# Optimization experiments

Measured on AMD Instinct MI355X. Metric: run time of the kernel, lower is better.

## Reference

```python
import jax, jax.numpy as jnp
import numpy as np

B, S, E, H = 4, 4096, 1024, 16
D = E // H  # head_dim = 64
EPS = 1e-6


def setup_inputs() -> dict:
    key = jax.random.key(0)
    ks = jax.random.split(key, 11)
    inv = 1.0 / np.sqrt(E)
    return {
        "query": jax.random.normal(ks[0], (B, S, E), dtype=jnp.float32),
        "key": jax.random.normal(ks[1], (B, S, E), dtype=jnp.float32),
        "value": jax.random.normal(ks[2], (B, S, E), dtype=jnp.float32),
        "key_padding_mask": jnp.zeros((B, S), dtype=bool),
        "Wq": jax.random.uniform(ks[3], (E, E), jnp.float32, -inv, inv),
        "bq": jnp.zeros((E,), jnp.float32),
        "Wk": jax.random.uniform(ks[4], (E, E), jnp.float32, -inv, inv),
        "bk": jnp.zeros((E,), jnp.float32),
        "Wv": jax.random.uniform(ks[5], (E, E), jnp.float32, -inv, inv),
        "bv": jnp.zeros((E,), jnp.float32),
        "Wo": jax.random.uniform(ks[6], (E, E), jnp.float32, -inv, inv),
        "bo": jnp.zeros((E,), jnp.float32),
    }


def _heads(x):
    # (B,S,E) -> (B,H,S,D)
    return x.reshape(B, -1, H, D).transpose(0, 2, 1, 3)


def reference(query, key, value, key_padding_mask, Wq, bq, Wk, bk, Wv, bv, Wo, bo):
    q = _heads(query @ Wq.T + bq)
    k = _heads(key @ Wk.T + bk)
    v = _heads(value @ Wv.T + bv)

    q_aug = jax.nn.relu(q) + EPS
    k_aug = jax.nn.relu(k) + EPS
    # mask out padded keys: (B,S_k) -> (B,1,S_k,1)
    k_aug = jnp.where(key_padding_mask[:, None, :, None], 0.0, k_aug)

    kv_context = jnp.einsum("bhsd,bhsv->bhdv", k_aug, v)  # (B,H,D,D)
    k_sum = k_aug.sum(axis=2)                                # (B,H,D)
    denom = jnp.einsum("bhqd,bhd->bhq", q_aug, k_sum)
    denom = jnp.maximum(denom, EPS)

    attn = jnp.einsum("bhqd,bhdv->bhqv", q_aug, kv_context) / denom[..., None]
    attn = attn.transpose(0, 2, 1, 3).reshape(B, -1, E)      # (B,S_q,E)
    # dropout is identity in eval mode
    return attn @ Wo.T + bo
```

## Files before the change

### kernel.cpp

```cpp
#include <hip/hip_runtime.h>
#include <hip/hip_bf16.h>
#include <stdint.h>

#define B_ 4
#define S_ 4096
#define E_ 1024
#define H_ 16
#define D_ 64
#define M_ (B_*S_)
constexpr float kEPS = 1e-6f;

typedef unsigned short u16;
typedef unsigned char  u8;
typedef __bf16 bf16x8 __attribute__((ext_vector_type(8)));
typedef float  f32x4  __attribute__((ext_vector_type(4)));
typedef u16    u16x8  __attribute__((ext_vector_type(8)));

typedef const __attribute__((address_space(1))) void* gaddr_t;
typedef __attribute__((address_space(3))) void*       laddr_t;

__device__ __forceinline__ u16 f2bf(float f) {
    union { float f; uint32_t u; } v; v.f = f;
    uint32_t u = v.u;
    u += 0x7fffu + ((u >> 16) & 1u);
    return (u16)(u >> 16);
}
__device__ __forceinline__ float hi2f(uint32_t d) {
    union { uint32_t u; float f; } v; v.u = d & 0xffff0000u;
    return v.f;
}
__device__ __forceinline__ float lo2f(uint32_t d) {
    union { uint32_t u; float f; } v; v.u = d << 16;
    return v.f;
}

#define VM_WAIT(n) asm volatile("s_waitcnt vmcnt(" #n ")" ::: "memory")
#define LG0        asm volatile("s_waitcnt lgkmcnt(0)" ::: "memory")
#define SBAR       asm volatile("s_barrier" ::: "memory")

__global__ __launch_bounds__(256)
void cvt3_kernel(const float* __restrict__ s0, const float* __restrict__ s1,
                 const float* __restrict__ s2,
                 u16* __restrict__ d0, u16* __restrict__ d1, u16* __restrict__ d2,
                 int n4)
{
    const int z = blockIdx.y;
    const float* src = (z == 0) ? s0 : (z == 1) ? s1 : s2;
    u16*         dst = (z == 0) ? d0 : (z == 1) ? d1 : d2;
    const int stride = gridDim.x * blockDim.x;
    for (int i = blockIdx.x * blockDim.x + threadIdx.x; i < n4; i += stride) {
        float4 v = reinterpret_cast<const float4*>(src)[i];
        ushort4 o;
        o.x = f2bf(v.x); o.y = f2bf(v.y); o.z = f2bf(v.z); o.w = f2bf(v.w);
        reinterpret_cast<ushort4*>(dst)[i] = o;
    }
}

__global__ __launch_bounds__(256)
void cvtw_kernel(const float* __restrict__ w0, const float* __restrict__ w1,
                 const float* __restrict__ w2, const float* __restrict__ w3,
                 u16* __restrict__ o0, u16* __restrict__ o1,
                 u16* __restrict__ o2, u16* __restrict__ o3)
{
    const int z = blockIdx.y;
    const float* src = (z == 0) ? w0 : (z == 1) ? w1 : (z == 2) ? w2 : w3;
    u16*         dst = (z == 0) ? o0 : (z == 1) ? o1 : (z == 2) ? o2 : o3;
    const int i = blockIdx.x * blockDim.x + threadIdx.x;
    float4 v = reinterpret_cast<const float4*>(src)[i];
    ushort4 o;
    o.x = f2bf(v.x); o.y = f2bf(v.y); o.z = f2bf(v.z); o.w = f2bf(v.w);
    reinterpret_cast<ushort4*>(dst)[i] = o;
}

#define BM2 256
#define BN2 128
#define BKT2 32
#define NT2 (E_/BKT2)

struct QKVArgs {
    const u16*   A[3];
    const u16*   W[3];
    const float* bias[3];
    const u8*    mask;
    u16*         C[3];
};

template<bool MERGED>
__global__ __launch_bounds__(512, 4)
void gemm2b(QKVArgs qa,
            const u16* __restrict__ A1, const u16* __restrict__ Bw1,
            const float* __restrict__ bias1, float* __restrict__ Cf)
{
    extern __shared__ u16 lds[];
    const int tid  = threadIdx.x;
    const int wid  = tid >> 6, lane = tid & 63;
    const int wqr  = wid >> 1, wqc = wid & 1;
    const int m0   = blockIdx.x * BM2;
    const int n0   = blockIdx.y * BN2;
    const int fr   = lane & 15;
    const int cg   = lane >> 4;

    const u16* A;  const u16* Bw;  const float* bias;  u16* Cb;  int epi;
    if constexpr (MERGED) {
        const int z = blockIdx.z;
        A = qa.A[z]; Bw = qa.W[z]; bias = qa.bias[z]; Cb = qa.C[z]; epi = z + 1;
    } else {
        A = A1; Bw = Bw1; bias = bias1; Cb = nullptr; epi = 0;
    }

    const int srow = tid >> 2;
    const int skey = (srow ^ (srow >> 2)) & 3;
    const int sck  = (tid & 3) ^ skey;
    const u16* aS0 = A  + (size_t)(m0 + srow)*E_        + sck*8;
    const u16* aS1 = A  + (size_t)(m0 + 128 + srow)*E_  + sck*8;
    const u16* bS0 = Bw + (size_t)(n0 + srow)*E_        + sck*8;

    const int lkey = (fr ^ (fr >> 2)) & 3;
    const int kxr  = (cg ^ lkey) * 8;
    int arow[4], brow[4];
#pragma unroll
    for (int mf = 0; mf < 4; ++mf) arow[mf] = (wqr*64 + mf*16 + fr)*32 + kxr;
#pragma unroll
    for (int nf = 0; nf < 4; ++nf) brow[nf] = 8192 + (wqc*64 + nf*16 + fr)*32 + kxr;

    f32x4 acc[4][4] = {};

    float bias_v[4];
#pragma unroll
    for (int nf = 0; nf < 4; ++nf) bias_v[nf] = bias[n0 + wqc*64 + nf*16 + fr];

#define STAGE(BUF, T) do { \
        const size_t ko_ = (size_t)(T) * BKT2; \
        u16* ab_ = lds + (BUF)*12288; \
        __builtin_amdgcn_global_load_lds((gaddr_t)(aS0 + ko_), (laddr_t)(ab_ + tid*8),          16, 0, 0); \
        __builtin_amdgcn_global_load_lds((gaddr_t)(aS1 + ko_), (laddr_t)(ab_ + (tid+512)*8),    16, 0, 0); \
        __builtin_amdgcn_global_load_lds((gaddr_t)(bS0 + ko_), (laddr_t)(ab_ + 8192 + tid*8),   16, 0, 0); \
    } while (0)

    STAGE(0, 0);
    VM_WAIT(0);
    SBAR;
    __builtin_amdgcn_sched_barrier(0);

#pragma unroll 1
    for (int T = 0; T < NT2; ++T) {
        const int cb = T & 1;
        const u16* buf = lds + cb*12288;
        bf16x8 afr[4], bfv[4];
#pragma unroll
        for (int mf = 0; mf < 4; ++mf) afr[mf] = *reinterpret_cast<const bf16x8*>(buf + arow[mf]);
#pragma unroll
        for (int nf = 0; nf < 4; ++nf) bfv[nf] = *reinterpret_cast<const bf16x8*>(buf + brow[nf]);
        if (T < NT2 - 1) STAGE(cb ^ 1, T + 1);
        LG0;
        __builtin_amdgcn_sched_barrier(0);
        __builtin_amdgcn_s_setprio(1);
#pragma unroll
        for (int mf = 0; mf < 4; ++mf)
#pragma unroll
            for (int nf = 0; nf < 4; ++nf)
                acc[mf][nf] = __builtin_amdgcn_mfma_f32_16x16x32_bf16(afr[mf], bfv[nf], acc[mf][nf], 0, 0, 0);
        __builtin_amdgcn_s_setprio(0);
        VM_WAIT(0);
        SBAR;
        __builtin_amdgcn_sched_barrier(0);
    }
#undef STAGE

    const int bblk = m0 >> 12;
    const int sloc = m0 & 4095;
#pragma unroll
    for (int mf = 0; mf < 4; ++mf) {
#pragma unroll
        for (int nf = 0; nf < 4; ++nf) {
            const int gn = n0 + wqc*64 + nf*16 + fr;
            const int mb = wqr*64 + mf*16 + cg*4;
            if (epi >= 2) {
                ushort4 o;
#pragma unroll
                for (int r = 0; r < 4; ++r) {
                    float x = acc[mf][nf][r] + bias_v[nf];
                    if (epi == 2) {
                        x = fmaxf(x, 0.f) + kEPS;
                        if (qa.mask[m0 + mb + r]) x = 0.f;
                    }
                    ((u16*)&o)[r] = f2bf(x);
                }
                *reinterpret_cast<ushort4*>(Cb + ((size_t)(bblk*1024 + gn))*4096 + sloc + mb) = o;
            } else if (epi == 1) {
#pragma unroll
                for (int r = 0; r < 4; ++r) {
                    const int gm = m0 + mb + r;
                    float x = acc[mf][nf][r] + bias_v[nf];
                    x = fmaxf(x, 0.f) + kEPS;
                    Cb[(size_t)gm*E_ + gn] = f2bf(x);
                }
            } else {
#pragma unroll
                for (int r = 0; r < 4; ++r) {
                    const int gm = m0 + mb + r;
                    Cf[(size_t)gm*E_ + gn] = acc[mf][nf][r] + bias_v[nf];
                }
            }
        }
    }
}

#define NSC 8
#define KCH (S_/NSC)
__global__ __launch_bounds__(256)
void kv_mfma_kernel(const u16* __restrict__ KaT, const u16* __restrict__ VvT,
                    float* __restrict__ kvp, float* __restrict__ ksp)
{
    __shared__ float sm[4][64];
    const int bh = blockIdx.x, sc = blockIdx.y;
    const int tid = threadIdx.x;
    const int w = tid >> 6, lane = tid & 63;
    const int fr = lane & 15, cg = lane >> 4;

    const u16* Ar = VvT + ((size_t)bh*64 + w*16 + fr)*4096 + sc*KCH;
    const u16* Br0 = KaT + ((size_t)bh*64 + fr)*4096 + sc*KCH;

    f32x4 acc[4] = {};
#pragma unroll 2
    for (int ks = 0; ks < KCH/32; ++ks) {
        const int ko = ks*32 + cg*8;
        bf16x8 af = *reinterpret_cast<const bf16x8*>(Ar + ko);
#pragma unroll
        for (int nf = 0; nf < 4; ++nf) {
            bf16x8 bf = *reinterpret_cast<const bf16x8*>(Br0 + (size_t)nf*16*4096 + ko);
            acc[nf] = __builtin_amdgcn_mfma_f32_16x16x32_bf16(af, bf, acc[nf], 0, 0, 0);
        }
    }
    float* dst = kvp + ((size_t)sc*64 + bh)*4096;
#pragma unroll
    for (int nf = 0; nf < 4; ++nf)
#pragma unroll
        for (int r = 0; r < 4; ++r)
            dst[(w*16 + cg*4 + r)*64 + nf*16 + fr] = acc[nf][r];

    {
        const int d = tid & 63, qq = tid >> 6;
        const u16* kr = KaT + ((size_t)bh*64 + d)*4096 + sc*KCH + qq*(KCH/4);
        float s = 0.f;
#pragma unroll 4
        for (int i = 0; i < KCH/4/8; ++i) {
            bf16x8 kk = *reinterpret_cast<const bf16x8*>(kr + i*8);
#pragma unroll
            for (int j = 0; j < 8; ++j) s += (float)kk[j];
        }
        sm[qq][d] = s;
    }
    __syncthreads();
    if (tid < 64)
        ksp[((size_t)sc*64 + bh)*64 + tid] = sm[0][tid] + sm[1][tid] + sm[2][tid] + sm[3][tid];
}

__global__ __launch_bounds__(256)
void kv_reduce_kernel(const float* __restrict__ kvp, const float* __restrict__ ksp,
                      u16* __restrict__ kvT, float* __restrict__ ksum)
{
    const int i = blockIdx.x*256 + threadIdx.x;
    float s = 0.f;
#pragma unroll
    for (int c = 0; c < NSC; ++c) s += kvp[(size_t)c*262144 + i];
    kvT[i] = f2bf(s);
    if (i < 4096) {
        float t = 0.f;
#pragma unroll
        for (int c = 0; c < NSC; ++c) t += ksp[(size_t)c*4096 + i];
        ksum[i] = t;
    }
}

__global__ __launch_bounds__(256)
void attn_kernel(const u16* __restrict__ Qa, const u16* __restrict__ kvT,
                 const float* __restrict__ ksum, u16* __restrict__ attn)
{
    __shared__ u16  Qs[256*64];
    __shared__ u16  Ts[64*64];
    __shared__ float kss[64];
    __shared__ float invd[256];

    const int bh = blockIdx.x, b = bh >> 4, h = bh & 15;
    const int s0 = blockIdx.y * 256;
    const int tid = threadIdx.x;
    const int wid = tid >> 6, lane = tid & 63;
    const int fr = lane & 15, cg = lane >> 4;

#pragma unroll
    for (int j = 0; j < 8; ++j) {
        int L = (wid*8 + j)*64 + lane;
        int row = L >> 3, c = L & 7;
        int cs = c ^ (row & 7);
        const u16* src = Qa + (size_t)(b*S_ + s0 + row)*E_ + h*64 + cs*8;
        __builtin_amdgcn_global_load_lds((gaddr_t)src, (laddr_t)(Qs + L*8), 16, 0, 0);
    }
#pragma unroll
    for (int k = 0; k < 2; ++k) {
        int g = k*256 + tid;
        int v = g >> 3, c = g & 7;
        uint4 q = *reinterpret_cast<const uint4*>(kvT + (size_t)bh*4096 + g*8);
        int cs = c ^ (v & 7);
        *reinterpret_cast<uint4*>(Ts + v*64 + cs*8) = q;
    }
    if (tid < 64) kss[tid] = ksum[bh*64 + tid];
    asm volatile("s_waitcnt vmcnt(0) lgkmcnt(0)" ::: "memory");
    __syncthreads();

    {
        float den = 0.f;
#pragma unroll
        for (int c = 0; c < 8; ++c) {
            uint4 qc = *reinterpret_cast<const uint4*>(Qs + tid*64 + (c ^ (tid & 7))*8);
            den += lo2f(qc.x)*kss[c*8+0] + hi2f(qc.x)*kss[c*8+1]
                 + lo2f(qc.y)*kss[c*8+2] + hi2f(qc.y)*kss[c*8+3]
                 + lo2f(qc.z)*kss[c*8+4] + hi2f(qc.z)*kss[c*8+5]
                 + lo2f(qc.w)*kss[c*8+6] + hi2f(qc.w)*kss[c*8+7];
        }
        invd[tid] = 1.0f / fmaxf(den, kEPS);
    }
    __syncthreads();

    f32x4 acc[4][4] = {};
#pragma unroll
    for (int ks = 0; ks < 2; ++ks) {
        bf16x8 bfrag[4];
#pragma unroll
        for (int nf = 0; nf < 4; ++nf) {
            int v = nf*16 + fr;
            bfrag[nf] = *reinterpret_cast<const bf16x8*>(Ts + v*64 + ((ks*4 + cg) ^ (v & 7))*8);
        }
#pragma unroll
        for (int mf = 0; mf < 4; ++mf) {
            int m = wid*64 + mf*16 + fr;
            bf16x8 afrag = *reinterpret_cast<const bf16x8*>(Qs + m*64 + ((ks*4 + cg) ^ (m & 7))*8);
#pragma unroll
            for (int nf = 0; nf < 4; ++nf)
                acc[mf][nf] = __builtin_amdgcn_mfma_f32_16x16x32_bf16(afrag, bfrag[nf], acc[mf][nf], 0, 0, 0);
        }
    }

#pragma unroll
    for (int mf = 0; mf < 4; ++mf) {
#pragma unroll
        for (int nf = 0; nf < 4; ++nf) {
            const int v = nf*16 + fr;
#pragma unroll
            for (int r = 0; r < 4; ++r) {
                const int row = wid*64 + mf*16 + cg*4 + r;
                float x = acc[mf][nf][r] * invd[row];
                attn[(size_t)(b*S_ + s0 + row)*E_ + h*64 + v] = f2bf(x);
            }
        }
    }
}

extern "C" void kernel_launch(void* const* d_in, const int* in_sizes, int n_in,
                              void* d_out, int out_size, void* d_ws, size_t ws_size,
                              hipStream_t stream)
{
    const float* query = (const float*)d_in[0];
    const float* key   = (const float*)d_in[1];
    const float* value = (const float*)d_in[2];
    const u8*    mask  = (const u8*)d_in[3];
    const float* Wq = (const float*)d_in[4];
    const float* bq = (const float*)d_in[5];
    const float* Wk = (const float*)d_in[6];
    const float* bk = (const float*)d_in[7];
    const float* Wv = (const float*)d_in[8];
    const float* bv = (const float*)d_in[9];
    const float* Wo = (const float*)d_in[10];
    const float* bo = (const float*)d_in[11];
    float* out = (float*)d_out;

    const size_t SZ_ME = (size_t)M_ * E_;
    const size_t SZ_EE = (size_t)E_ * E_;

    char* ws = (char*)d_ws;
    u16* qx   = (u16*)ws; ws += SZ_ME*2;
    u16* kx   = (u16*)ws; ws += SZ_ME*2;
    u16* vx   = (u16*)ws; ws += SZ_ME*2;
    u16* Qa   = (u16*)ws; ws += SZ_ME*2;
    u16* KaT  = (u16*)ws; ws += SZ_ME*2;
    u16* VvT  = (u16*)ws; ws += SZ_ME*2;
    u16* wqb  = (u16*)ws; ws += SZ_EE*2;
    u16* wkb  = (u16*)ws; ws += SZ_EE*2;
    u16* wvb  = (u16*)ws; ws += SZ_EE*2;
    u16* wob  = (u16*)ws; ws += SZ_EE*2;
    float* kvp = (float*)ws; ws += (size_t)NSC*64*4096*4;
    float* ksp = (float*)ws; ws += (size_t)NSC*4096*4;
    u16*  kvT  = (u16*)ws;  ws += (size_t)64*4096*2;
    float* ksum= (float*)ws; ws += 4096*4;

    u16* attnb = qx;

    cvt3_kernel<<<dim3(2048, 3), 256, 0, stream>>>(query, key, value, qx, kx, vx, (int)(SZ_ME/4));
    cvtw_kernel<<<dim3(1024, 4), 256, 0, stream>>>(Wq, Wk, Wv, Wo, wqb, wkb, wvb, wob);

    QKVArgs qa;
    qa.A[0] = qx;  qa.A[1] = kx;  qa.A[2] = vx;
    qa.W[0] = wqb; qa.W[1] = wkb; qa.W[2] = wvb;
    qa.bias[0] = bq; qa.bias[1] = bk; qa.bias[2] = bv;
    qa.mask = mask;
    qa.C[0] = Qa; qa.C[1] = KaT; qa.C[2] = VvT;
    dim3 ggrid(M_/BM2, E_/BN2, 3);
    constexpr size_t LDS_BYTES = 2 * 12288 * sizeof(u16);
    gemm2b<true><<<ggrid, 512, LDS_BYTES, stream>>>(qa, nullptr, nullptr, nullptr, nullptr);

    kv_mfma_kernel<<<dim3(64, NSC), 256, 0, stream>>>(KaT, VvT, kvp, ksp);
    kv_reduce_kernel<<<1024, 256, 0, stream>>>(kvp, ksp, kvT, ksum);

    attn_kernel<<<dim3(B_*H_, S_/256), 256, 0, stream>>>(Qa, kvT, ksum, attnb);

    QKVArgs dummy = {};
    dummy.mask = mask;
    gemm2b<false><<<dim3(M_/BM2, E_/BN2, 1), 512, LDS_BYTES, stream>>>(dummy, attnb, wob, bo, out);
}
```

Measured before the change: 279.9 us.

## Retile projection GEMMs to 128x128 tiles with 64-deep K and 8-way swizzle

```diff
diff --git a/kernel.cpp b/kernel.cpp
--- a/kernel.cpp
+++ b/kernel.cpp
@@ -72,10 +72,10 @@
     reinterpret_cast<ushort4*>(dst)[i] = o;
 }
 
-#define BM2 256
-#define BN2 128
-#define BKT2 32
-#define NT2 (E_/BKT2)
+#define BM 128
+#define BN 128
+#define BKT 64
+#define NKT (E_/BKT)
 
 struct QKVArgs {
     const u16*   A[3];
@@ -86,17 +86,17 @@
 };
 
 template<bool MERGED>
-__global__ __launch_bounds__(512, 4)
-void gemm2b(QKVArgs qa,
-            const u16* __restrict__ A1, const u16* __restrict__ Bw1,
-            const float* __restrict__ bias1, float* __restrict__ Cf)
+__global__ __launch_bounds__(256, 2)
+void gemm128(QKVArgs qa,
+             const u16* __restrict__ A1, const u16* __restrict__ Bw1,
+             const float* __restrict__ bias1, float* __restrict__ Cf)
 {
     extern __shared__ u16 lds[];
     const int tid  = threadIdx.x;
     const int wid  = tid >> 6, lane = tid & 63;
     const int wqr  = wid >> 1, wqc = wid & 1;
-    const int m0   = blockIdx.x * BM2;
-    const int n0   = blockIdx.y * BN2;
+    const int m0   = blockIdx.x * BM;
+    const int n0   = blockIdx.y * BN;
     const int fr   = lane & 15;
     const int cg   = lane >> 4;
 
@@ -108,20 +108,21 @@
         A = A1; Bw = Bw1; bias = bias1; Cb = nullptr; epi = 0;
     }
 
-    const int srow = tid >> 2;
-    const int skey = (srow ^ (srow >> 2)) & 3;
-    const int sck  = (tid & 3) ^ skey;
-    const u16* aS0 = A  + (size_t)(m0 + srow)*E_        + sck*8;
-    const u16* aS1 = A  + (size_t)(m0 + 128 + srow)*E_  + sck*8;
-    const u16* bS0 = Bw + (size_t)(n0 + srow)*E_        + sck*8;
-
-    const int lkey = (fr ^ (fr >> 2)) & 3;
-    const int kxr  = (cg ^ lkey) * 8;
+    int srowj[4], sckj[4];
+#pragma unroll
+    for (int j = 0; j < 4; ++j) {
+        const int s = j*256 + tid;
+        srowj[j] = s >> 3;
+        sckj[j]  = (s & 7) ^ (srowj[j] & 7);
+    }
+
     int arow[4], brow[4];
 #pragma unroll
-    for (int mf = 0; mf < 4; ++mf) arow[mf] = (wqr*64 + mf*16 + fr)*32 + kxr;
-#pragma unroll
-    for (int nf = 0; nf < 4; ++nf) brow[nf] = 8192 + (wqc*64 + nf*16 + fr)*32 + kxr;
+    for (int mf = 0; mf < 4; ++mf) arow[mf] = (wqr*64 + mf*16 + fr)*64;
+#pragma unroll
+    for (int nf = 0; nf < 4; ++nf) brow[nf] = 8192 + (wqc*64 + nf*16 + fr)*64;
+    const int kx0 = ((cg)     ^ (fr & 7)) * 8;
+    const int kx1 = ((4 + cg) ^ (fr & 7)) * 8;
 
     f32x4 acc[4][4] = {};
 
@@ -130,11 +131,15 @@
     for (int nf = 0; nf < 4; ++nf) bias_v[nf] = bias[n0 + wqc*64 + nf*16 + fr];
 
 #define STAGE(BUF, T) do { \
-        const size_t ko_ = (size_t)(T) * BKT2; \
-        u16* ab_ = lds + (BUF)*12288; \
-        __builtin_amdgcn_global_load_lds((gaddr_t)(aS0 + ko_), (laddr_t)(ab_ + tid*8),          16, 0, 0); \
-        __builtin_amdgcn_global_load_lds((gaddr_t)(aS1 + ko_), (laddr_t)(ab_ + (tid+512)*8),    16, 0, 0); \
-        __builtin_amdgcn_global_load_lds((gaddr_t)(bS0 + ko_), (laddr_t)(ab_ + 8192 + tid*8),   16, 0, 0); \
+        const size_t ko_ = (size_t)(T) * BKT; \
+        u16* lb_ = lds + (BUF)*16384; \
+        _Pragma("unroll") \
+        for (int j_ = 0; j_ < 4; ++j_) { \
+            const u16* as_ = A  + (size_t)(m0 + srowj[j_])*E_ + ko_ + sckj[j_]*8; \
+            const u16* bs_ = Bw + (size_t)(n0 + srowj[j_])*E_ + ko_ + sckj[j_]*8; \
+            __builtin_amdgcn_global_load_lds((gaddr_t)as_, (laddr_t)(lb_ + (j_*256 + tid)*8),        16, 0, 0); \
+            __builtin_amdgcn_global_load_lds((gaddr_t)bs_, (laddr_t)(lb_ + 8192 + (j_*256 + tid)*8), 16, 0, 0); \
+        } \
     } while (0)
 
     STAGE(0, 0);
@@ -143,23 +148,31 @@
     __builtin_amdgcn_sched_barrier(0);
 
 #pragma unroll 1
-    for (int T = 0; T < NT2; ++T) {
+    for (int T = 0; T < NKT; ++T) {
         const int cb = T & 1;
-        const u16* buf = lds + cb*12288;
-        bf16x8 afr[4], bfv[4];
-#pragma unroll
-        for (int mf = 0; mf < 4; ++mf) afr[mf] = *reinterpret_cast<const bf16x8*>(buf + arow[mf]);
-#pragma unroll
-        for (int nf = 0; nf < 4; ++nf) bfv[nf] = *reinterpret_cast<const bf16x8*>(buf + brow[nf]);
-        if (T < NT2 - 1) STAGE(cb ^ 1, T + 1);
+        const u16* buf = lds + cb*16384;
+        bf16x8 afr[4][2], bfv[4][2];
+#pragma unroll
+        for (int mf = 0; mf < 4; ++mf) {
+            afr[mf][0] = *reinterpret_cast<const bf16x8*>(buf + arow[mf] + kx0);
+            afr[mf][1] = *reinterpret_cast<const bf16x8*>(buf + arow[mf] + kx1);
+        }
+#pragma unroll
+        for (int nf = 0; nf < 4; ++nf) {
+            bfv[nf][0] = *reinterpret_cast<const bf16x8*>(buf + brow[nf] + kx0);
+            bfv[nf][1] = *reinterpret_cast<const bf16x8*>(buf + brow[nf] + kx1);
+        }
+        if (T < NKT - 1) STAGE(cb ^ 1, T + 1);
         LG0;
         __builtin_amdgcn_sched_barrier(0);
         __builtin_amdgcn_s_setprio(1);
 #pragma unroll
         for (int mf = 0; mf < 4; ++mf)
 #pragma unroll
-            for (int nf = 0; nf < 4; ++nf)
-                acc[mf][nf] = __builtin_amdgcn_mfma_f32_16x16x32_bf16(afr[mf], bfv[nf], acc[mf][nf], 0, 0, 0);
+            for (int nf = 0; nf < 4; ++nf) {
+                acc[mf][nf] = __builtin_amdgcn_mfma_f32_16x16x32_bf16(afr[mf][0], bfv[nf][0], acc[mf][nf], 0, 0, 0);
+                acc[mf][nf] = __builtin_amdgcn_mfma_f32_16x16x32_bf16(afr[mf][1], bfv[nf][1], acc[mf][nf], 0, 0, 0);
+            }
         __builtin_amdgcn_s_setprio(0);
         VM_WAIT(0);
         SBAR;
@@ -404,9 +417,9 @@
     qa.bias[0] = bq; qa.bias[1] = bk; qa.bias[2] = bv;
     qa.mask = mask;
     qa.C[0] = Qa; qa.C[1] = KaT; qa.C[2] = VvT;
-    dim3 ggrid(M_/BM2, E_/BN2, 3);
-    constexpr size_t LDS_BYTES = 2 * 12288 * sizeof(u16);
-    gemm2b<true><<<ggrid, 512, LDS_BYTES, stream>>>(qa, nullptr, nullptr, nullptr, nullptr);
+    dim3 ggrid(M_/BM, E_/BN, 3);
+    constexpr size_t LDS_BYTES = 2 * 16384 * sizeof(u16);
+    gemm128<true><<<ggrid, 256, LDS_BYTES, stream>>>(qa, nullptr, nullptr, nullptr, nullptr);
 
     kv_mfma_kernel<<<dim3(64, NSC), 256, 0, stream>>>(KaT, VvT, kvp, ksp);
     kv_reduce_kernel<<<1024, 256, 0, stream>>>(kvp, ksp, kvT, ksum);
@@ -415,5 +428,5 @@
 
     QKVArgs dummy = {};
     dummy.mask = mask;
-    gemm2b<false><<<dim3(M_/BM2, E_/BN2, 1), 512, LDS_BYTES, stream>>>(dummy, attnb, wob, bo, out);
-}
+    gemm128<false><<<dim3(M_/BM, E_/BN, 1), 256, LDS_BYTES, stream>>>(dummy, attnb, wob, bo, out);
+}
```

Measured after the change: 283.5 us. No clear change (+1.3%).
